# Kernel tuning notes

Hardware: AMD Instinct MI355X
Metric: run time of the kernel (lower is better)

## Reference

```python
import jax, jax.numpy as jnp
from jax import lax
import numpy as np

B, T, TW, EW = 32, 64, 32, 300   # dialogues, utterances, words, word-embed
H = 512                          # lstm hidden per direction
E = 2 * H                        # utterance embedding size
HH = 512                         # emotion hidden size
C = 7                            # output classes


def setup_inputs() -> dict:
    key = jax.random.key(0)
    ks = jax.random.split(key, 24)
    n = lambda k, shp: (jax.random.normal(k, shp, dtype=jnp.float32) * 0.05)
    inp = {
        "input_data": jax.random.normal(ks[0], (B, T, TW, EW), dtype=jnp.float32),
        # BiLSTM (torch gate order i,f,g,o)
        "lstm_Wih_f": n(ks[1], (4 * H, EW)), "lstm_Whh_f": n(ks[2], (4 * H, H)), "lstm_b_f": n(ks[3], (4 * H,)),
        "lstm_Wih_b": n(ks[4], (4 * H, EW)), "lstm_Whh_b": n(ks[5], (4 * H, H)), "lstm_b_b": n(ks[6], (4 * H,)),
        # attention weight
        "W_att": n(ks[7], (E, E)),
        # global-state GRUCell (torch gate order r,z,n)
        "g_Wih": n(ks[8], (3 * E, E)), "g_Whh": n(ks[9], (3 * E, E)), "g_bih": n(ks[10], (3 * E,)), "g_bhh": n(ks[11], (3 * E,)),
        # party-state GRUCell
        "p_Wih": n(ks[12], (3 * E, E)), "p_Whh": n(ks[13], (3 * E, E)), "p_bih": n(ks[14], (3 * E,)), "p_bhh": n(ks[15], (3 * E,)),
        # emotion-state GRUCell (input E, hidden HH)
        "e_Wih": n(ks[16], (3 * HH, E)), "e_Whh": n(ks[17], (3 * HH, HH)), "e_bih": n(ks[18], (3 * HH,)), "e_bhh": n(ks[19], (3 * HH,)),
        # classifier
        "cls_W": n(ks[20], (C, HH)), "cls_b": n(ks[21], (C,)),
    }
    return inp


def _gru_cell(x, h, Wih, Whh, bih, bhh):
    gi = x @ Wih.T + bih
    gh = h @ Whh.T + bhh
    ir, iz, inn = jnp.split(gi, 3, axis=-1)
    hr, hz, hn = jnp.split(gh, 3, axis=-1)
    r = jax.nn.sigmoid(ir + hr)
    z = jax.nn.sigmoid(iz + hz)
    n = jnp.tanh(inn + r * hn)
    return (1.0 - z) * n + z * h


def _lstm_last_hidden(xs, Wih, Whh, b):
    # xs: [Tw, N, Ew] -> final hidden [N, H]
    N = xs.shape[1]
    h0 = jnp.zeros((N, H), xs.dtype)

    def step(carry, x):
        h, c = carry
        g = x @ Wih.T + h @ Whh.T + b
        i_, f_, g_, o_ = jnp.split(g, 4, axis=-1)
        c2 = jax.nn.sigmoid(f_) * c + jax.nn.sigmoid(i_) * jnp.tanh(g_)
        h2 = jax.nn.sigmoid(o_) * jnp.tanh(c2)
        return (h2, c2), None

    (h, _), _ = lax.scan(step, (h0, h0), xs)
    return h


def _forward(input_data, lstm_Wih_f, lstm_Whh_f, lstm_b_f, lstm_Wih_b, lstm_Whh_b, lstm_b_b,
             W_att, g_Wih, g_Whh, g_bih, g_bhh, p_Wih, p_Whh, p_bih, p_bhh,
             e_Wih, e_Whh, e_bih, e_bhh, cls_W, cls_b):
    # ---- FeatureExtraction: BiLSTM over words, take fwd-last + bwd-first hidden ----
    x = input_data.reshape(B * T, TW, EW).transpose(1, 0, 2)          # [Tw, N, Ew]
    h_fwd = _lstm_last_hidden(x, lstm_Wih_f, lstm_Whh_f, lstm_b_f)     # [N, H]
    h_bwd = _lstm_last_hidden(x[::-1], lstm_Wih_b, lstm_Whh_b, lstm_b_b)  # [N, H]
    feats = jnp.concatenate([h_fwd, h_bwd], axis=-1).reshape(B, T, E)  # [B, T, 2H]

    # ---- EmotionDetection: sequential recurrence over utterances ----
    utt = feats.transpose(1, 0, 2)                                     # [T, B, E]
    hist0 = jnp.zeros((T + 1, B, E), feats.dtype)   # global_state history (idx 0 = zero init)
    party0 = jnp.zeros((2, B, E), feats.dtype)
    emo0 = jnp.zeros((B, HH), feats.dtype)
    l_idx = jnp.arange(T + 1)[:, None]              # [T+1, 1]

    def step(carry, inp):
        hist, party, emo = carry
        x_i, i = inp
        p = i % 2
        g_prev = hist[i]                                               # global_state[i]
        new_g = _gru_cell(x_i + party[p], g_prev, g_Wih, g_Whh, g_bih, g_bhh)
        hist = hist.at[i + 1].set(new_g)
        # attention over history indices 0..i (excludes the just-appended state)
        q = x_i @ W_att                                                # [B, E]
        scores = jnp.einsum('be,lbe->lb', q, hist)                     # [T+1, B]
        scores = jnp.where(l_idx <= i, scores, -jnp.inf)
        w = jax.nn.softmax(scores, axis=0)[:, :, None]                 # [T+1, B, 1]
        context = jnp.sum(hist * w, axis=0)                            # [B, E]
        new_p = _gru_cell(x_i + context, party[p], p_Wih, p_Whh, p_bih, p_bhh)
        party = party.at[p].set(new_p)
        emo = _gru_cell(new_p, emo, e_Wih, e_Whh, e_bih, e_bhh)        # [B, HH]
        return (hist, party, emo), emo

    _, emo_seq = lax.scan(step, (hist0, party0, emo0), (utt, jnp.arange(T)))
    emo_seq = emo_seq.transpose(1, 0, 2)                               # [B, T, HH]
    return emo_seq @ cls_W.T + cls_b                                   # [B, T, C]


def reference(input_data, lstm_Wih_f, lstm_Whh_f, lstm_b_f, lstm_Wih_b, lstm_Whh_b, lstm_b_b,
              W_att, g_Wih, g_Whh, g_bih, g_bhh, p_Wih, p_Whh, p_bih, p_bhh,
              e_Wih, e_Whh, e_bih, e_bhh, cls_W, cls_b):
    return _forward(input_data, lstm_Wih_f, lstm_Whh_f, lstm_b_f, lstm_Wih_b, lstm_Whh_b, lstm_b_b,
                    W_att, g_Wih, g_Whh, g_bih, g_bhh, p_Wih, p_Whh, p_bih, p_bhh,
                    e_Wih, e_Whh, e_bih, e_bhh, cls_W, cls_b)
```

## Files before the change

kernel.cpp:

```cpp
#include <hip/hip_runtime.h>
#include <math.h>

#define B_  32
#define T_  64
#define TW_ 32
#define EW_ 300
#define H_  512
#define E_  1024
#define HH_ 512
#define C_  7
#define N_  2048

typedef float f32x4 __attribute__((ext_vector_type(4)));
typedef short s16x8 __attribute__((ext_vector_type(8)));
typedef unsigned short u16;
typedef unsigned int u32;

__device__ __forceinline__ float sigm(float x){ return 1.f/(1.f+expf(-x)); }
__device__ __forceinline__ float bf2f(u16 u){
  union{float f; unsigned v;} x; x.v = ((unsigned)u)<<16; return x.f;
}
__device__ __forceinline__ u16 f2bf(float f){
  union{float f; unsigned v;} x; x.f = f;
  unsigned r = x.v + 0x7FFF + ((x.v>>16)&1);
  return (u16)(r>>16);
}
__device__ __forceinline__ void g2lds16(const void* g, void* l){
  __builtin_amdgcn_global_load_lds((const __attribute__((address_space(1))) u32*)g,
                                   (__attribute__((address_space(3))) u32*)l, 16, 0, 0);
}

__global__ __launch_bounds__(256) void k_pack_lstm(
    const float* __restrict__ Wih_f, const float* __restrict__ Whh_f,
    const float* __restrict__ Wih_b, const float* __restrict__ Whh_b,
    u16* __restrict__ Wpack2)
{
  size_t idx = (size_t)blockIdx.x*256 + threadIdx.x;
  if(idx >= (size_t)4096*832) return;
  int k   = (int)(idx % 832);
  int row = (int)(idx / 832);
  int p   = row & 127;
  int pan = row >> 7;
  int dir = pan >> 4, mt = pan & 15;
  int g = p >> 5, ml = p & 31;
  int R = g*512 + mt*32 + ml;
  const float* Wih = dir ? Wih_b : Wih_f;
  const float* Whh = dir ? Whh_b : Whh_f;
  float v = (k < 320) ? ((k < EW_) ? Wih[(size_t)R*EW_ + k] : 0.f)
                      : Whh[(size_t)R*H_ + (k-320)];
  Wpack2[idx] = f2bf(v);
}

__global__ __launch_bounds__(256) void k_f2bf(const float* __restrict__ src,
                                              u16* __restrict__ dst, int n)
{
  int idx = blockIdx.x*256 + threadIdx.x;
  if(idx < n) dst[idx] = f2bf(src[idx]);
}

__global__ __launch_bounds__(256) void k_wattT(const float* __restrict__ W,
                                               u16* __restrict__ dst)
{
  int idx = blockIdx.x*256 + threadIdx.x;
  if(idx >= E_*E_) return;
  int j = idx >> 10, k = idx & 1023;
  dst[idx] = f2bf(W[(size_t)k*E_ + j]);
}

__global__ __launch_bounds__(256) void lstm2(
    const float* __restrict__ xin, const u16* __restrict__ Wpack2,
    const float* __restrict__ b_f, const float* __restrict__ b_b,
    const u16* __restrict__ hbf_in, u16* __restrict__ hbf_out,
    float* __restrict__ cb, u16* __restrict__ featsbf, int t)
{
  const int panel = blockIdx.x;
  const int dir = panel & 1, mt = panel >> 1;
  const int n0 = blockIdx.y * 128;
  const int wt = dir ? (TW_-1-t) : t;
  const u16* Wpan = Wpack2 + (size_t)(dir*16+mt)*128*832;
  const u16* hin_d = hbf_in + (size_t)dir*N_*H_;

  __shared__ __align__(16) u16 As[2][128*32];
  __shared__ __align__(16) u16 Bs[2][128*32];

  const int tid = threadIdx.x;
  const int w = tid >> 6, l = tid & 63;
  const int lr = l & 15, lh = l >> 4;
  const int wn = w >> 1, wm = w & 1;
  const int xrow = tid >> 1, khalf = (tid & 1)*16;

  f32x4 acc[4][4];
  #pragma unroll
  for(int a=0;a<4;a++)
    #pragma unroll
    for(int g=0;g<4;g++) acc[a][g] = (f32x4){0.f,0.f,0.f,0.f};

  auto issueW = [&](int kc, int b){
    #pragma unroll
    for(int c=0;c<2;++c){
      const int cc = w*2 + c;
      const char* g = (const char*)Wpan + (size_t)(cc*16 + (l>>2))*1664 + kc*64 + (l&3)*16;
      g2lds16(g, (char*)&Bs[b][0] + cc*1024);
    }
  };
  auto issueAh = [&](int kc, int b){
    #pragma unroll
    for(int c=0;c<2;++c){
      const int cc = w*2 + c;
      const char* g = (const char*)hin_d + (size_t)(n0 + cc*16 + (l>>2))*1024 + (kc-10)*64 + (l&3)*16;
      g2lds16(g, (char*)&As[b][0] + cc*1024);
    }
  };
  auto loadXx = [&](int kc, float4* xv4){
    const float* xs = xin + ((size_t)(n0 + xrow)*TW_ + wt)*EW_;
    const int gk = kc*32 + khalf;
    #pragma unroll
    for(int j=0;j<4;++j){
      const int k = gk + j*4;
      if(k + 3 < EW_) xv4[j] = *(const float4*)&xs[k];
      else {
        float4 tmp = {0.f,0.f,0.f,0.f};
        if(k   < EW_) tmp.x = xs[k];
        if(k+1 < EW_) tmp.y = xs[k+1];
        if(k+2 < EW_) tmp.z = xs[k+2];
        xv4[j] = tmp;
      }
    }
  };
  auto finishXx = [&](const float4* xv4, int b){
    const float* xf = (const float*)xv4;
    s16x8 o0, o1;
    #pragma unroll
    for(int j=0;j<8;++j){ o0[j] = (short)f2bf(xf[j]); o1[j] = (short)f2bf(xf[8+j]); }
    *(s16x8*)&As[b][xrow*32 + khalf]     = o0;
    *(s16x8*)&As[b][xrow*32 + khalf + 8] = o1;
  };

  {
    issueW(0, 0);
    float4 xv4[4];
    loadXx(0, xv4);
    finishXx(xv4, 0);
  }
  __syncthreads();

  for(int kc=0; kc<26; ++kc){
    const int cur = kc & 1, nxt = cur ^ 1;
    const int kn = kc + 1;
    float4 xv4[4];
    const bool prex = (kn < 10);
    if(kn < 26){
      issueW(kn, nxt);
      if(prex) loadXx(kn, xv4);
      else     issueAh(kn, nxt);
    }
    s16x8 av[4], bv[4];
    #pragma unroll
    for(int nf=0; nf<4; ++nf)
      av[nf] = *(const s16x8*)&As[cur][(wn*64 + nf*16 + lr)*32 + lh*8];
    #pragma unroll
    for(int g=0; g<4; ++g)
      bv[g] = *(const s16x8*)&Bs[cur][(g*32 + wm*16 + lr)*32 + lh*8];
    #pragma unroll
    for(int g=0; g<4; ++g)
      #pragma unroll
      for(int nf=0; nf<4; ++nf)
        acc[nf][g] = __builtin_amdgcn_mfma_f32_16x16x32_bf16(av[nf], bv[g], acc[nf][g], 0,0,0);
    if(prex) finishXx(xv4, nxt);
    __syncthreads();
  }

  const float* bias = dir ? b_b : b_f;
  const int m = mt*32 + wm*16 + lr;
  const float bi = bias[m], bfv = bias[H_+m], bg = bias[2*H_+m], bo = bias[3*H_+m];
  float* cbp = cb + (size_t)dir*N_*H_;
  u16* ho = hbf_out + (size_t)dir*N_*H_;
  #pragma unroll
  for(int nf=0; nf<4; ++nf){
    #pragma unroll
    for(int r=0; r<4; ++r){
      const int n = n0 + wn*64 + nf*16 + lh*4 + r;
      float gi = acc[nf][0][r] + bi;
      float gf = acc[nf][1][r] + bfv;
      float gc = acc[nf][2][r] + bg;
      float go = acc[nf][3][r] + bo;
      float c_old = cbp[(size_t)n*H_ + m];
      float c2 = sigm(gf)*c_old + sigm(gi)*tanhf(gc);
      float h2 = sigm(go)*tanhf(c2);
      cbp[(size_t)n*H_ + m] = c2;
      if(t == TW_-1) featsbf[(size_t)n*E_ + dir*H_ + m] = f2bf(h2);
      else           ho[(size_t)n*H_ + m] = f2bf(h2);
    }
  }
}

__global__ __launch_bounds__(256) void k_qgemm(const u16* __restrict__ featsbf,
                                               const u16* __restrict__ WattT,
                                               float* __restrict__ q)
{
  const int n0 = blockIdx.x*64, j0 = blockIdx.y*64;
  __shared__ __align__(16) u16 As[64*40];
  __shared__ __align__(16) u16 Bs[64*40];
  const int tid = threadIdx.x;
  const int w = tid>>6, l = tid&63, lr = l&15, lk = (l>>4)*8;
  const int arow = tid>>2, ak8 = (tid&3)*8;

  f32x4 acc[4];
  #pragma unroll
  for(int i=0;i<4;i++) acc[i] = (f32x4){0.f,0.f,0.f,0.f};

  for(int kc=0; kc<32; ++kc){
    *(s16x8*)&As[arow*40 + ak8] = *(const s16x8*)&featsbf[(size_t)(n0+arow)*E_ + kc*32 + ak8];
    *(s16x8*)&Bs[arow*40 + ak8] = *(const s16x8*)&WattT[(size_t)(j0+arow)*E_ + kc*32 + ak8];
    __syncthreads();
    s16x8 av = *(const s16x8*)&As[(w*16 + lr)*40 + lk];
    #pragma unroll
    for(int mf=0; mf<4; ++mf){
      s16x8 bv = *(const s16x8*)&Bs[(mf*16 + lr)*40 + lk];
      acc[mf] = __builtin_amdgcn_mfma_f32_16x16x32_bf16(av, bv, acc[mf], 0,0,0);
    }
    __syncthreads();
  }
  #pragma unroll
  for(int mf=0; mf<4; ++mf)
    #pragma unroll
    for(int r=0; r<4; ++r){
      int n = n0 + w*16 + (l>>4)*4 + r;
      q[(size_t)n*E_ + j0 + mf*16 + lr] = acc[mf][r];
    }
}

struct GArg2 {
  const u16* xA; const u16* xB;
  long ldA; long ldB;
  const u16* W; int K;
};

__device__ __forceinline__ void gemm32v2(const GArg2 a, int R, int xt, int ks,
                                         int KS, int z, float* __restrict__ part,
                                         char* smem)
{
  u16* Xs0 = (u16*)smem;
  u16* Xs1 = Xs0 + 32*40;
  u16* Ws0 = Xs1 + 32*40;
  u16* Ws1 = Ws0 + 128*32;
  const int Kc = a.K / KS;
  const int nch = Kc >> 5;
  const int kb0 = ks * Kc;
  const int tid = threadIdx.x;
  const int w = tid>>6, l = tid&63, lr = l&15, lh = l>>4;

  f32x4 a00={0,0,0,0}, a01={0,0,0,0}, a10={0,0,0,0}, a11={0,0,0,0};

  auto issueW = [&](int c, u16* Wb){
    const int kb = kb0 + c*32;
    #pragma unroll
    for(int c2=0;c2<2;++c2){
      const int cc = w*2 + c2;
      const char* g = (const char*)(a.W + (size_t)(xt*128 + cc*16 + (l>>2))*a.K + kb) + (l&3)*16;
      g2lds16(g, (char*)Wb + cc*1024);
    }
  };
  auto loadX = [&](int c, short4* xr){
    const int kb = kb0 + c*32;
    const int row = tid>>3, k4 = (tid&7)*4;
    short4 xv = *(const short4*)&a.xA[(size_t)row*a.ldA + kb + k4];
    if(a.xB){
      short4 yv = *(const short4*)&a.xB[(size_t)row*a.ldB + kb + k4];
      xv.x = (short)f2bf(bf2f((u16)xv.x)+bf2f((u16)yv.x));
      xv.y = (short)f2bf(bf2f((u16)xv.y)+bf2f((u16)yv.y));
      xv.z = (short)f2bf(bf2f((u16)xv.z)+bf2f((u16)yv.z));
      xv.w = (short)f2bf(bf2f((u16)xv.w)+bf2f((u16)yv.w));
    }
    *xr = xv;
  };
  auto writeX = [&](short4 xv, u16* Xb){
    *(short4*)&Xb[(tid>>3)*40 + (tid&7)*4] = xv;
  };

  short4 xr;
  issueW(0, Ws0); loadX(0, &xr); writeX(xr, Xs0);
  __syncthreads();
  for(int c=0;c<nch;++c){
    u16* Xc = (c&1)?Xs1:Xs0; u16* Wc = (c&1)?Ws1:Ws0;
    u16* Xn = (c&1)?Xs0:Xs1; u16* Wn = (c&1)?Ws0:Ws1;
    const bool pre = (c+1 < nch);
    if(pre){ issueW(c+1, Wn); loadX(c+1, &xr); }
    s16x8 av0 = *(const s16x8*)&Xc[lr*40 + lh*8];
    s16x8 av1 = *(const s16x8*)&Xc[(16+lr)*40 + lh*8];
    s16x8 bv0 = *(const s16x8*)&Wc[(w*32 + lr)*32 + lh*8];
    s16x8 bv1 = *(const s16x8*)&Wc[(w*32 + 16 + lr)*32 + lh*8];
    a00 = __builtin_amdgcn_mfma_f32_16x16x32_bf16(av0, bv0, a00, 0,0,0);
    a01 = __builtin_amdgcn_mfma_f32_16x16x32_bf16(av0, bv1, a01, 0,0,0);
    a10 = __builtin_amdgcn_mfma_f32_16x16x32_bf16(av1, bv0, a10, 0,0,0);
    a11 = __builtin_amdgcn_mfma_f32_16x16x32_bf16(av1, bv1, a11, 0,0,0);
    if(pre) writeX(xr, Xn);
    __syncthreads();
  }
  float* dst = part + (size_t)((z*KS + ks)*B_)*R + xt*128 + w*32;
  f32x4 accs[2][2] = {{a00,a01},{a10,a11}};
  #pragma unroll
  for(int nf=0; nf<2; ++nf)
    #pragma unroll
    for(int mf=0; mf<2; ++mf)
      #pragma unroll
      for(int r=0; r<4; ++r){
        int n = nf*16 + lh*4 + r;
        dst[(size_t)n*R + mf*16 + lr] = accs[nf][mf][r];
      }
}

__device__ __forceinline__ void att_body(const float* __restrict__ q,
                                         const u16* __restrict__ histbf,
                                         const u16* __restrict__ featsbf,
                                         u16* __restrict__ xcbf,
                                         int i, int b, char* smem)
{
  float* qs = (float*)smem;
  float* sc = qs + E_;
  const int tid = threadIdx.x;
  *(float4*)&qs[tid*4] = *(const float4*)&q[((size_t)b*T_ + i)*E_ + tid*4];
  __syncthreads();
  const int wv = tid>>6, ln = tid&63;
  for(int L = wv; L <= i; L += 4){
    const u16* hl = histbf + ((size_t)L*B_ + b)*E_;
    float s = 0.f;
    s16x8 h0 = *(const s16x8*)&hl[ln*16];
    s16x8 h1 = *(const s16x8*)&hl[ln*16 + 8];
    #pragma unroll
    for(int j=0;j<8;j++){
      s += qs[ln*16 + j]     * bf2f((u16)h0[j]);
      s += qs[ln*16 + 8 + j] * bf2f((u16)h1[j]);
    }
    #pragma unroll
    for(int off=32; off; off>>=1) s += __shfl_down(s, off);
    if(ln == 0) sc[L] = s;
  }
  __syncthreads();
  if(tid < 64){
    float v  = (tid <= i) ? sc[tid] : -INFINITY;
    float mx = v;
    #pragma unroll
    for(int off=32; off; off>>=1) mx = fmaxf(mx, __shfl_xor(mx, off));
    float ex = (tid <= i) ? expf(v - mx) : 0.f;
    float sm = ex;
    #pragma unroll
    for(int off=32; off; off>>=1) sm += __shfl_xor(sm, off);
    sc[tid] = ex / sm;
  }
  __syncthreads();
  const int e4 = tid*4;
  float c0=0.f, c1=0.f, c2=0.f, c3=0.f;
  for(int L=0; L<=i; ++L){
    float wl = sc[L];
    short4 hv = *(const short4*)&histbf[((size_t)L*B_ + b)*E_ + e4];
    c0 += wl*bf2f((u16)hv.x);
    c1 += wl*bf2f((u16)hv.y);
    c2 += wl*bf2f((u16)hv.z);
    c3 += wl*bf2f((u16)hv.w);
  }
  const u16* xi = featsbf + ((size_t)b*T_ + i)*E_ + e4;
  xcbf[(size_t)b*E_ + e4 + 0] = f2bf(bf2f(xi[0]) + c0);
  xcbf[(size_t)b*E_ + e4 + 1] = f2bf(bf2f(xi[1]) + c1);
  xcbf[(size_t)b*E_ + e4 + 2] = f2bf(bf2f(xi[2]) + c2);
  xcbf[(size_t)b*E_ + e4 + 3] = f2bf(bf2f(xi[3]) + c3);
}

__device__ __forceinline__ void gru_comb(const float* __restrict__ part, int R, int J, int KS,
                                         const float* __restrict__ bih, const float* __restrict__ bhh,
                                         const float* __restrict__ hprev_f,
                                         float* __restrict__ dst_f,
                                         u16* __restrict__ dstbf,
                                         float* __restrict__ dst_seq, int idx)
{
  const int b = idx / J, e = idx - b*J;
  float ir=0.f, iz=0.f, in_=0.f, hr=0.f, hz=0.f, hn=0.f;
  for(int ks=0; ks<KS; ++ks){
    const float* p0 = part + (size_t)(ks*B_ + b)*R;
    const float* p1 = part + (size_t)((KS+ks)*B_ + b)*R;
    ir += p0[e]; iz += p0[J+e]; in_ += p0[2*J+e];
    hr += p1[e]; hz += p1[J+e]; hn  += p1[2*J+e];
  }
  ir += bih[e]; iz += bih[J+e]; in_ += bih[2*J+e];
  hr += bhh[e]; hz += bhh[J+e]; hn  += bhh[2*J+e];
  const float r = sigm(ir + hr);
  const float z = sigm(iz + hz);
  const float n = tanhf(in_ + r*hn);
  const float hp = hprev_f[(size_t)b*J + e];
  const float h2 = (1.f - z)*n + z*hp;
  dst_f[(size_t)b*J + e] = h2;
  dstbf[(size_t)b*J + e] = f2bf(h2);
  if(dst_seq) dst_seq[(size_t)b*J + e] = h2;
}

__global__ __launch_bounds__(256) void k_A(GArg2 g0, GArg2 g1, GArg2 e0, GArg2 e1,
    float* __restrict__ part_g, float* __restrict__ part_e,
    const float* __restrict__ q, const u16* __restrict__ histbf,
    const u16* __restrict__ featsbf, u16* __restrict__ xcbf, int i)
{
  __shared__ __align__(16) char smem[21504];
  const int x = blockIdx.x;
  if(x < 384){
    if(i >= T_) return;
    const int xt = x % 24, ks = (x/24) & 7, z = x/192;
    gemm32v2(z ? g1 : g0, 3*E_, xt, ks, 8, z, part_g, smem);
  } else if(x < 576){
    if(i < 1) return;
    const int ix = x-384, xt = ix % 12, ks = (ix/12) & 7, z = ix/96;
    gemm32v2(z ? e1 : e0, 3*HH_, xt, ks, 8, z, part_e, smem);
  } else {
    if(i >= T_) return;
    att_body(q, histbf, featsbf, xcbf, i, x-576, smem);
  }
}

__global__ __launch_bounds__(256) void k_B(GArg2 p0, GArg2 p1,
    const float* __restrict__ part_g, const float* __restrict__ part_e,
    const float* __restrict__ g_bih, const float* __restrict__ g_bhh,
    const float* __restrict__ e_bih, const float* __restrict__ e_bhh,
    const float* __restrict__ gf_prev, float* __restrict__ gf_next,
    u16* __restrict__ histbf,
    float* __restrict__ emof, u16* __restrict__ emobf,
    float* __restrict__ emo_seq, float* __restrict__ part_p, int i)
{
  __shared__ __align__(16) char smem[21504];
  const int x = blockIdx.x;
  if(x < 128){
    if(i >= T_) return;
    gru_comb(part_g, 3*E_, E_, 8, g_bih, g_bhh,
             gf_prev, gf_next, histbf + (size_t)(i+1)*B_*E_, nullptr,
             x*256 + (int)threadIdx.x);
  } else if(x < 512){
    if(i >= T_) return;
    const int ix = x-128, xt = ix % 24, ks = (ix/24) & 7, z = ix/192;
    gemm32v2(z ? p1 : p0, 3*E_, xt, ks, 8, z, part_p, smem);
  } else {
    if(i < 1) return;
    gru_comb(part_e, 3*HH_, HH_, 8, e_bih, e_bhh,
             emof, emof, emobf, emo_seq + (size_t)(i-1)*B_*HH_,
             (x-512)*256 + (int)threadIdx.x);
  }
}

__global__ __launch_bounds__(256) void k_C(const float* __restrict__ part_p,
    const float* __restrict__ p_bih, const float* __restrict__ p_bhh,
    float* __restrict__ partyf_p, u16* __restrict__ partybf_p)
{
  const int idx = blockIdx.x*256 + threadIdx.x;
  gru_comb(part_p, 3*E_, E_, 8, p_bih, p_bhh, partyf_p, partyf_p, partybf_p, nullptr, idx);
}

__global__ __launch_bounds__(256) void classify(const float* __restrict__ emo_seq,
    const float* __restrict__ clsW, const float* __restrict__ clsb, float* __restrict__ out)
{
  const int idx = blockIdx.x*256 + threadIdx.x;
  if(idx >= B_*T_*C_) return;
  const int c = idx % C_;
  const int bt = idx / C_;
  const int t = bt % T_, b = bt / T_;
  const float* e = emo_seq + (size_t)(t*B_ + b)*HH_;
  const float* w = clsW + (size_t)c*HH_;
  float s = clsb[c];
  for(int h=0; h<HH_; ++h) s += e[h]*w[h];
  out[idx] = s;
}

extern "C" void kernel_launch(void* const* d_in, const int* in_sizes, int n_in,
                              void* d_out, int out_size, void* d_ws, size_t ws_size,
                              hipStream_t stream)
{
  const float* input  = (const float*)d_in[0];
  const float* Wih_f  = (const float*)d_in[1];
  const float* Whh_f  = (const float*)d_in[2];
  const float* b_f    = (const float*)d_in[3];
  const float* Wih_b  = (const float*)d_in[4];
  const float* Whh_b  = (const float*)d_in[5];
  const float* b_b    = (const float*)d_in[6];
  const float* W_att  = (const float*)d_in[7];
  const float* g_Wih  = (const float*)d_in[8];
  const float* g_Whh  = (const float*)d_in[9];
  const float* g_bih  = (const float*)d_in[10];
  const float* g_bhh  = (const float*)d_in[11];
  const float* p_Wih  = (const float*)d_in[12];
  const float* p_Whh  = (const float*)d_in[13];
  const float* p_bih  = (const float*)d_in[14];
  const float* p_bhh  = (const float*)d_in[15];
  const float* e_Wih  = (const float*)d_in[16];
  const float* e_Whh  = (const float*)d_in[17];
  const float* e_bih  = (const float*)d_in[18];
  const float* e_bhh  = (const float*)d_in[19];
  const float* cls_W  = (const float*)d_in[20];
  const float* cls_b  = (const float*)d_in[21];

  char* base = (char*)d_ws;
  size_t off = 0;
  auto alloc = [&](size_t bytes)->char*{
    char* p = base + off; off += (bytes + 255) & ~(size_t)255; return p;
  };
  u16*   Wpack2  = (u16*)alloc((size_t)4096*832*2);
  u16*   hbfA    = (u16*)alloc((size_t)2*N_*H_*2);
  u16*   hbfB    = (u16*)alloc((size_t)2*N_*H_*2);
  float* cb      = (float*)alloc((size_t)2*N_*H_*4);
  u16*   featsbf = (u16*)alloc((size_t)N_*E_*2);
  float* q       = (float*)alloc((size_t)N_*E_*4);
  u16*   WattT   = (u16*)alloc((size_t)E_*E_*2);
  u16*   gWih    = (u16*)alloc((size_t)3*E_*E_*2);
  u16*   gWhh    = (u16*)alloc((size_t)3*E_*E_*2);
  u16*   pWih    = (u16*)alloc((size_t)3*E_*E_*2);
  u16*   pWhh    = (u16*)alloc((size_t)3*E_*E_*2);
  u16*   eWih    = (u16*)alloc((size_t)3*HH_*E_*2);
  u16*   eWhh    = (u16*)alloc((size_t)3*HH_*HH_*2);
  u16*   histbf  = (u16*)alloc((size_t)(T_+1)*B_*E_*2);
  float* gfbuf   = (float*)alloc((size_t)2*B_*E_*4);
  float* partyf  = (float*)alloc((size_t)2*B_*E_*4);
  u16*   partybf = (u16*)alloc((size_t)2*B_*E_*2);
  float* emof    = (float*)alloc((size_t)B_*HH_*4);
  u16*   emobf   = (u16*)alloc((size_t)B_*HH_*2);
  float* emo_seq = (float*)alloc((size_t)T_*B_*HH_*4);
  u16*   xcbf    = (u16*)alloc((size_t)B_*E_*2);
  float* part_e  = (float*)alloc((size_t)16*B_*3*HH_*4);
  float* part_g  = (float*)cb;
  float* part_p  = (float*)hbfA;

  hipMemsetAsync(hbfA,    0, (size_t)2*N_*H_*2, stream);
  hipMemsetAsync(cb,      0, (size_t)2*N_*H_*4, stream);
  hipMemsetAsync(histbf,  0, (size_t)B_*E_*2, stream);
  hipMemsetAsync(gfbuf,   0, (size_t)B_*E_*4, stream);
  hipMemsetAsync(partyf,  0, (size_t)2*B_*E_*4, stream);
  hipMemsetAsync(partybf, 0, (size_t)2*B_*E_*2, stream);
  hipMemsetAsync(emof,    0, (size_t)B_*HH_*4, stream);
  hipMemsetAsync(emobf,   0, (size_t)B_*HH_*2, stream);

  k_pack_lstm<<<dim3(((size_t)4096*832+255)/256), 256, 0, stream>>>(Wih_f, Whh_f, Wih_b, Whh_b, Wpack2);
  k_f2bf<<<dim3((3*E_*E_+255)/256), 256, 0, stream>>>(g_Wih, gWih, 3*E_*E_);
  k_f2bf<<<dim3((3*E_*E_+255)/256), 256, 0, stream>>>(g_Whh, gWhh, 3*E_*E_);
  k_f2bf<<<dim3((3*E_*E_+255)/256), 256, 0, stream>>>(p_Wih, pWih, 3*E_*E_);
  k_f2bf<<<dim3((3*E_*E_+255)/256), 256, 0, stream>>>(p_Whh, pWhh, 3*E_*E_);
  k_f2bf<<<dim3((3*HH_*E_+255)/256), 256, 0, stream>>>(e_Wih, eWih, 3*HH_*E_);
  k_f2bf<<<dim3((3*HH_*HH_+255)/256), 256, 0, stream>>>(e_Whh, eWhh, 3*HH_*HH_);
  k_wattT<<<dim3((E_*E_+255)/256), 256, 0, stream>>>(W_att, WattT);

  for(int t=0; t<TW_; ++t){
    u16* hin  = (t & 1) ? hbfB : hbfA;
    u16* hout = (t & 1) ? hbfA : hbfB;
    lstm2<<<dim3(32, 16), 256, 0, stream>>>(input, Wpack2, b_f, b_b,
                                            hin, hout, cb, featsbf, t);
  }

  k_qgemm<<<dim3(32, 16), 256, 0, stream>>>(featsbf, WattT, q);

  for(int i=0; i<=T_; ++i){
    const int p  = i & 1;
    const int pe = (i-1) & 1;
    GArg2 ga0{ featsbf + (size_t)i*E_, partybf + (size_t)p*B_*E_, (long)T_*E_, (long)E_, gWih, E_ };
    GArg2 ga1{ histbf + (size_t)i*B_*E_, nullptr, (long)E_, 0, gWhh, E_ };
    GArg2 ea0{ partybf + (size_t)pe*B_*E_, nullptr, (long)E_, 0, eWih, E_ };
    GArg2 ea1{ emobf, nullptr, (long)HH_, 0, eWhh, HH_ };
    k_A<<<dim3(608), 256, 0, stream>>>(ga0, ga1, ea0, ea1, part_g, part_e,
                                       q, histbf, featsbf, xcbf, i);
    GArg2 pa0{ xcbf, nullptr, (long)E_, 0, pWih, E_ };
    GArg2 pa1{ partybf + (size_t)p*B_*E_, nullptr, (long)E_, 0, pWhh, E_ };
    k_B<<<dim3(576), 256, 0, stream>>>(pa0, pa1, part_g, part_e,
                                       g_bih, g_bhh, e_bih, e_bhh,
                                       gfbuf + (size_t)(i&1)*B_*E_,
                                       gfbuf + (size_t)((i+1)&1)*B_*E_,
                                       histbf, emof, emobf, emo_seq, part_p, i);
    if(i < T_){
      k_C<<<dim3(128), 256, 0, stream>>>(part_p, p_bih, p_bhh,
                                         partyf + (size_t)p*B_*E_,
                                         partybf + (size_t)p*B_*E_);
    }
  }

  classify<<<dim3((B_*T_*C_+255)/256), 256, 0, stream>>>(emo_seq, cls_W, cls_b, (float*)d_out);
}
```

Measured before the change: 2.920 ms.

## Triple-buffer LSTM step GEMM with prefetch distance two and manual waitcnt barriers

Reworks the per-timestep LSTM GEMM kernel from double to triple LDS buffering. Weight and hidden-state tiles are now issued two k-chunks ahead, and syncthreads is replaced with explicit s_waitcnt vmcnt(4) plus s_barrier. The loop is fully unrolled so that async global-to-LDS latency overlaps with MFMA work. This costs 50% more LDS per block, which may lower occupancy, and the hand-set vmcnt counts must match the number of loads in flight.

```diff
diff --git a/kernel.cpp b/kernel.cpp
--- a/kernel.cpp
+++ b/kernel.cpp
@@ -67,7 +67,7 @@
   dst[idx] = f2bf(W[(size_t)k*E_ + j]);
 }
 
-__global__ __launch_bounds__(256) void lstm2(
+__global__ __launch_bounds__(256) void lstm2b(
     const float* __restrict__ xin, const u16* __restrict__ Wpack2,
     const float* __restrict__ b_f, const float* __restrict__ b_b,
     const u16* __restrict__ hbf_in, u16* __restrict__ hbf_out,
@@ -80,8 +80,8 @@
   const u16* Wpan = Wpack2 + (size_t)(dir*16+mt)*128*832;
   const u16* hin_d = hbf_in + (size_t)dir*N_*H_;
 
-  __shared__ __align__(16) u16 As[2][128*32];
-  __shared__ __align__(16) u16 Bs[2][128*32];
+  __shared__ __align__(16) u16 As[3][128*32];
+  __shared__ __align__(16) u16 Bs[3][128*32];
 
   const int tid = threadIdx.x;
   const int w = tid >> 6, l = tid & 63;
@@ -95,20 +95,20 @@
     #pragma unroll
     for(int g=0;g<4;g++) acc[a][g] = (f32x4){0.f,0.f,0.f,0.f};
 
-  auto issueW = [&](int kc, int b){
+  auto issueW = [&](int kc, u16* Bb){
     #pragma unroll
     for(int c=0;c<2;++c){
       const int cc = w*2 + c;
       const char* g = (const char*)Wpan + (size_t)(cc*16 + (l>>2))*1664 + kc*64 + (l&3)*16;
-      g2lds16(g, (char*)&Bs[b][0] + cc*1024);
-    }
-  };
-  auto issueAh = [&](int kc, int b){
+      g2lds16(g, (char*)Bb + cc*1024);
+    }
+  };
+  auto issueAh = [&](int kc, u16* Ab){
     #pragma unroll
     for(int c=0;c<2;++c){
       const int cc = w*2 + c;
       const char* g = (const char*)hin_d + (size_t)(n0 + cc*16 + (l>>2))*1024 + (kc-10)*64 + (l&3)*16;
-      g2lds16(g, (char*)&As[b][0] + cc*1024);
+      g2lds16(g, (char*)Ab + cc*1024);
     }
   };
   auto loadXx = [&](int kc, float4* xv4){
@@ -127,47 +127,49 @@
       }
     }
   };
-  auto finishXx = [&](const float4* xv4, int b){
+  auto finishXx = [&](const float4* xv4, u16* Ab){
     const float* xf = (const float*)xv4;
     s16x8 o0, o1;
     #pragma unroll
     for(int j=0;j<8;++j){ o0[j] = (short)f2bf(xf[j]); o1[j] = (short)f2bf(xf[8+j]); }
-    *(s16x8*)&As[b][xrow*32 + khalf]     = o0;
-    *(s16x8*)&As[b][xrow*32 + khalf + 8] = o1;
-  };
-
-  {
-    issueW(0, 0);
-    float4 xv4[4];
-    loadXx(0, xv4);
-    finishXx(xv4, 0);
-  }
-  __syncthreads();
-
+    *(s16x8*)&Ab[xrow*32 + khalf]     = o0;
+    *(s16x8*)&Ab[xrow*32 + khalf + 8] = o1;
+  };
+
+  float4 xv4[4];
+  loadXx(0, xv4);
+  issueW(0, &Bs[0][0]);
+  finishXx(xv4, &As[0][0]);
+  issueW(1, &Bs[1][0]);
+  loadXx(1, xv4);
+
+  #pragma unroll
   for(int kc=0; kc<26; ++kc){
-    const int cur = kc & 1, nxt = cur ^ 1;
-    const int kn = kc + 1;
-    float4 xv4[4];
-    const bool prex = (kn < 10);
-    if(kn < 26){
-      issueW(kn, nxt);
-      if(prex) loadXx(kn, xv4);
-      else     issueAh(kn, nxt);
-    }
+    if(kc < 25){
+      asm volatile("s_waitcnt vmcnt(4) lgkmcnt(0)\n\ts_barrier" ::: "memory");
+    } else {
+      asm volatile("s_waitcnt vmcnt(0) lgkmcnt(0)\n\ts_barrier" ::: "memory");
+    }
+    __builtin_amdgcn_sched_barrier(0);
+    const int cu = kc % 3, n1 = (kc+1) % 3, n2 = (kc+2) % 3;
+    if(kc+2 < 26){
+      issueW(kc+2, &Bs[n2][0]);
+      if(kc+2 >= 10) issueAh(kc+2, &As[n2][0]);
+    }
+    if(kc+1 < 10) finishXx(xv4, &As[n1][0]);
+    if(kc+2 < 10) loadXx(kc+2, xv4);
     s16x8 av[4], bv[4];
     #pragma unroll
     for(int nf=0; nf<4; ++nf)
-      av[nf] = *(const s16x8*)&As[cur][(wn*64 + nf*16 + lr)*32 + lh*8];
+      av[nf] = *(const s16x8*)&As[cu][(wn*64 + nf*16 + lr)*32 + lh*8];
     #pragma unroll
     for(int g=0; g<4; ++g)
-      bv[g] = *(const s16x8*)&Bs[cur][(g*32 + wm*16 + lr)*32 + lh*8];
+      bv[g] = *(const s16x8*)&Bs[cu][(g*32 + wm*16 + lr)*32 + lh*8];
     #pragma unroll
     for(int g=0; g<4; ++g)
       #pragma unroll
       for(int nf=0; nf<4; ++nf)
         acc[nf][g] = __builtin_amdgcn_mfma_f32_16x16x32_bf16(av[nf], bv[g], acc[nf][g], 0,0,0);
-    if(prex) finishXx(xv4, nxt);
-    __syncthreads();
   }
 
   const float* bias = dir ? b_b : b_f;
@@ -543,8 +545,8 @@
   for(int t=0; t<TW_; ++t){
     u16* hin  = (t & 1) ? hbfB : hbfA;
     u16* hout = (t & 1) ? hbfA : hbfB;
-    lstm2<<<dim3(32, 16), 256, 0, stream>>>(input, Wpack2, b_f, b_b,
-                                            hin, hout, cb, featsbf, t);
+    lstm2b<<<dim3(32, 16), 256, 0, stream>>>(input, Wpack2, b_f, b_b,
+                                             hin, hout, cb, featsbf, t);
   }
 
   k_qgemm<<<dim3(32, 16), 256, 0, stream>>>(featsbf, WattT, q);
```

Result: no change. 2.953 ms (+1.1%).
